# Optimization experiments

Hardware: AMD Instinct MI355X
Metric: run time of the kernel (lower is better)

Reference implementation:

```python
import jax, jax.numpy as jnp
import numpy as np

B, C, H, W = 8, 256, 128, 128
KC, VC, HEADS = 256, 256, 8


def setup_inputs() -> dict:
    key = jax.random.key(0)
    ks = jax.random.split(key, 10)
    s = 0.05
    return {
        "x": jax.random.normal(ks[0], (B, C, H, W), jnp.float32),
        "Wk": jax.random.normal(ks[1], (KC, C), jnp.float32) * s,
        "bk": jax.random.normal(ks[2], (KC,), jnp.float32) * s,
        "Wq": jax.random.normal(ks[3], (KC, C), jnp.float32) * s,
        "bq": jax.random.normal(ks[4], (KC,), jnp.float32) * s,
        "Wv": jax.random.normal(ks[5], (VC, C), jnp.float32) * s,
        "bv": jax.random.normal(ks[6], (VC,), jnp.float32) * s,
        "Wr": jax.random.normal(ks[7], (C, VC), jnp.float32) * s,
        "br": jax.random.normal(ks[8], (C,), jnp.float32) * s,
        "head_count": HEADS,
    }


def reference(x, Wk, bk, Wq, bq, Wv, bv, Wr, br, head_count):
    n, c, h, w = x.shape
    hw = h * w
    xf = x.reshape(n, c, hw)  # [n, C, S]
    # 1x1 convs == per-pixel linear projections
    keys = jnp.einsum('kc,ncs->nks', Wk, xf) + bk[None, :, None]
    queries = jnp.einsum('kc,ncs->nks', Wq, xf) + bq[None, :, None]
    values = jnp.einsum('vc,ncs->nvs', Wv, xf) + bv[None, :, None]

    dk = Wk.shape[0] // head_count
    dv = Wv.shape[0] // head_count
    # split heads along channel dim (matches torch channel slicing)
    K = jax.nn.softmax(keys.reshape(n, head_count, dk, hw), axis=-1)   # softmax over spatial
    Q = jax.nn.softmax(queries.reshape(n, head_count, dk, hw), axis=2) # softmax over key dim
    V = values.reshape(n, head_count, dv, hw)

    # context = K @ V^T : [n, h, dk, dv]
    ctx = jnp.einsum('nhks,nhvs->nhkv', K, V)
    # attended = ctx^T @ Q : [n, h, dv, S]
    att = jnp.einsum('nhkv,nhks->nhvs', ctx, Q).reshape(n, head_count * dv, h, w)

    attention = jnp.einsum('ov,nvhw->nohw', Wr, att) + br[None, :, None, None]
    # attention map: per-head mean over key dim, then mean over heads
    attention_map = K.mean(axis=2).mean(axis=1).reshape(n, h, w)
    # torch returns the LAST head's context (loop variable after the loop)
    context_last = ctx[:, -1]
    return attention, context_last, attention_map
```

## Files before the change

### kernel.cpp

```cpp
#include <hip/hip_runtime.h>
#include <hip/hip_bf16.h>

typedef float f32x4 __attribute__((ext_vector_type(4)));
typedef short s16x8 __attribute__((ext_vector_type(8)));
typedef short s16x4 __attribute__((ext_vector_type(4)));
typedef __bf16 bf16x8 __attribute__((ext_vector_type(8)));
typedef unsigned short u16;

#define DEVI __device__ __forceinline__

static constexpr int    HW      = 16384;
static constexpr size_t BSTRIDE = (size_t)256 * HW;

static constexpr size_t oXBT   = 0;
static constexpr size_t oEK    = oXBT  + (size_t)8 * HW * 256 * 2;
static constexpr size_t oQT    = oEK   + (size_t)8 * 256 * HW * 2;
static constexpr size_t oVB    = oQT   + (size_t)8 * HW * 256 * 2;
static constexpr size_t oWK    = oVB   + (size_t)8 * 256 * HW * 2;
static constexpr size_t oBIAS  = oWK   + (size_t)768 * 256 * 2;
static constexpr size_t oISE   = oBIAS + 4096;
static constexpr size_t oPS    = oISE  + 8192;
static constexpr size_t oCTX   = oPS   + (size_t)256 * 2048 * 4;
static constexpr size_t oMB    = oCTX  + (size_t)64 * 1024 * 4;
static constexpr size_t oCPART = oMB   + (size_t)8 * 256 * 256 * 2;
static constexpr size_t oMPART = oCPART + (size_t)4096 * 1024 * 4;

DEVI float bf2f(short x) {
  unsigned u = ((unsigned)(unsigned short)x) << 16;
  return __builtin_bit_cast(float, u);
}
DEVI u16 f2bf(float x) { return __builtin_bit_cast(u16, (__bf16)x); }

DEVI void gld16(const void* g, void* l) {
  __builtin_amdgcn_global_load_lds(
      (__attribute__((address_space(1))) void*)(g),
      (__attribute__((address_space(3))) void*)(l), 16, 0, 0);
}

__global__ __launch_bounds__(256) void k_pt(
    const float* __restrict__ x,
    const float* __restrict__ Wk, const float* __restrict__ Wq, const float* __restrict__ Wv,
    const float* __restrict__ bk, const float* __restrict__ bq, const float* __restrict__ bv,
    u16* __restrict__ xbT, u16* __restrict__ Wkqv, float* __restrict__ bias)
{
  __shared__ u16 lds[64 * 256];
  const int t = threadIdx.x;
  const int tb = blockIdx.x;
  if (tb < 2048) {
    const int n = tb >> 8;
    const int s0 = (tb & 255) * 64;
    const float* src = x + ((size_t)n * 256 + t) * HW + s0;
    #pragma unroll
    for (int i = 0; i < 16; ++i) {
      f32x4 v = *(const f32x4*)(src + i * 4);
      #pragma unroll
      for (int j = 0; j < 4; ++j) lds[(i * 4 + j) * 256 + t] = f2bf(v[j]);
    }
    __syncthreads();
    s16x8* gp = (s16x8*)(xbT + (size_t)n * BSTRIDE + (size_t)s0 * 256);
    const s16x8* lp = (const s16x8*)lds;
    #pragma unroll
    for (int i = 0; i < 8; ++i) gp[t + i * 256] = lp[t + i * 256];
  } else {
    const int i = (tb - 2048) * 256 + t;
    for (int p = i; p < 768 * 256; p += 64 * 256) {
      float v = (p < 65536) ? Wk[p] : (p < 131072 ? Wq[p - 65536] : Wv[p - 131072]);
      Wkqv[p] = f2bf(v);
    }
    if (i < 768) bias[i] = (i < 256) ? bk[i] : (i < 512 ? bq[i - 256] : bv[i - 512]);
  }
}

__global__ __launch_bounds__(256, 2) void k_proj3(
    const u16* __restrict__ W, const u16* __restrict__ xbT, const float* __restrict__ bias,
    u16* __restrict__ ek, u16* __restrict__ qT, u16* __restrict__ vb, float* __restrict__ ps)
{
  __shared__ u16 smem[40960];
  const int t = threadIdx.x;
  const int L = blockIdx.x;
  const int n = L & 7;
  const int idx = L >> 3;
  const int mh = idx & 1;
  const int sb = idx >> 1;
  const int m0 = mh * 128;
  const int s0 = sb * 128;
  const int lane = t & 63;
  const int l15 = lane & 15, l4 = (lane >> 4) & 3;
  const int wv = t >> 6;
  const int wm = (wv & 1) * 64, wn = (wv >> 1) * 64;

  const u16* Bb = xbT + (size_t)n * BSTRIDE + (size_t)s0 * 256;

  float bK[4], bV[4];
  #pragma unroll
  for (int mf = 0; mf < 4; ++mf) {
    bK[mf] = bias[m0 + wm + mf * 16 + l15];
    bV[mf] = bias[512 + m0 + wm + mf * 16 + l15];
  }

  #pragma unroll
  for (int i = 0; i < 16; ++i) {
    const int f = i * 256 + t;
    const int row = f >> 5, c = f & 31;
    gld16(Bb + (size_t)row * 256 + ((c ^ (row & 7)) * 8), smem + f * 8);
  }

  auto STAGEA = [&](int g) {
    const int kt = g & 7;
    const int op = g >> 3;
    const int wr0 = (op == 0) ? 0 : (op == 1 ? 512 : 256);
    const u16* Ab = W + (size_t)(wr0 + m0) * 256;
    #pragma unroll
    for (int i = 0; i < 2; ++i) {
      const int f = i * 256 + t;
      const int row = f >> 2, c = f & 3;
      gld16(Ab + (size_t)row * 256 + kt * 32 + ((c ^ (row & 3)) * 8),
            smem + 32768 + (g & 1) * 4096 + f * 8);
    }
  };

  STAGEA(0); STAGEA(1);

  f32x4 acc[4][4] = {};
  u16* ekb = ek + (size_t)n * BSTRIDE;
  u16* vbb = vb + (size_t)n * BSTRIDE;

  #pragma unroll
  for (int g = 0; g < 24; ++g) {
    if (g == 23) asm volatile("s_waitcnt vmcnt(0)" ::: "memory");
    else         asm volatile("s_waitcnt vmcnt(2)" ::: "memory");
    __builtin_amdgcn_s_barrier();

    const int kt = g & 7;
    bf16x8 af[4], bff[4];
    #pragma unroll
    for (int gg = 0; gg < 4; ++gg) {
      const int mrow = wm + gg * 16 + l15;
      const int srow = wn + gg * 16 + l15;
      const int cidx = kt * 4 + l4;
      af[gg]  = *(const bf16x8*)&smem[32768 + (g & 1) * 4096 + mrow * 32 + ((l4 ^ (mrow & 3)) * 8)];
      bff[gg] = *(const bf16x8*)&smem[srow * 256 + ((cidx ^ (srow & 7)) * 8)];
    }
    __builtin_amdgcn_s_setprio(1);
    if (g < 16) {
      #pragma unroll
      for (int sf = 0; sf < 4; ++sf)
        #pragma unroll
        for (int mf = 0; mf < 4; ++mf)
          acc[sf][mf] = __builtin_amdgcn_mfma_f32_16x16x32_bf16(bff[sf], af[mf], acc[sf][mf], 0, 0, 0);
    } else {
      #pragma unroll
      for (int mg = 0; mg < 4; ++mg)
        #pragma unroll
        for (int ng = 0; ng < 4; ++ng)
          acc[mg][ng] = __builtin_amdgcn_mfma_f32_16x16x32_bf16(af[mg], bff[ng], acc[mg][ng], 0, 0, 0);
    }
    __builtin_amdgcn_s_setprio(0);

    asm volatile("s_waitcnt lgkmcnt(0)" ::: "memory");
    __builtin_amdgcn_s_barrier();
    if (g < 22) STAGEA(g + 2);

    if (g == 7) {
      float rs[4] = {0.f, 0.f, 0.f, 0.f};
      #pragma unroll
      for (int sf = 0; sf < 4; ++sf)
        #pragma unroll
        for (int mf = 0; mf < 4; ++mf) {
          s16x4 pk;
          #pragma unroll
          for (int r = 0; r < 4; ++r) {
            const float e = __expf(acc[sf][mf][r] + bK[mf]);
            rs[mf] += e;
            pk[r] = (short)f2bf(e);
          }
          *(s16x4*)(ekb + (size_t)(m0 + wm + mf * 16 + l15) * HW + s0 + wn + sf * 16 + l4 * 4) = pk;
        }
      #pragma unroll
      for (int mf = 0; mf < 4; ++mf) {
        float v = rs[mf];
        v += __shfl_xor(v, 16); v += __shfl_xor(v, 32);
        if (l4 == 0)
          ps[((size_t)(sb * 2 + (wn >> 6))) * 2048 + n * 256 + m0 + wm + mf * 16 + l15] = v;
      }
      #pragma unroll
      for (int sf = 0; sf < 4; ++sf)
        #pragma unroll
        for (int mf = 0; mf < 4; ++mf) acc[sf][mf] = f32x4{0.f, 0.f, 0.f, 0.f};
    } else if (g == 15) {
      #pragma unroll
      for (int sf = 0; sf < 4; ++sf)
        #pragma unroll
        for (int mf = 0; mf < 4; ++mf) {
          s16x4 pk;
          #pragma unroll
          for (int r = 0; r < 4; ++r) pk[r] = (short)f2bf(acc[sf][mf][r] + bV[mf]);
          *(s16x4*)(vbb + (size_t)(m0 + wm + mf * 16 + l15) * HW + s0 + wn + sf * 16 + l4 * 4) = pk;
        }
      #pragma unroll
      for (int sf = 0; sf < 4; ++sf)
        #pragma unroll
        for (int mf = 0; mf < 4; ++mf) acc[sf][mf] = f32x4{0.f, 0.f, 0.f, 0.f};
    }
  }

  #pragma unroll
  for (int mg = 0; mg < 4; ++mg)
    #pragma unroll
    for (int r = 0; r < 4; ++r) {
      const float bb = bias[256 + m0 + wm + mg * 16 + l4 * 4 + r];
      #pragma unroll
      for (int ng = 0; ng < 4; ++ng) acc[mg][ng][r] += bb;
    }
  #pragma unroll
  for (int hh = 0; hh < 2; ++hh)
    #pragma unroll
    for (int ng = 0; ng < 4; ++ng) {
      float s = 0.f;
      #pragma unroll
      for (int mg = hh * 2; mg < hh * 2 + 2; ++mg)
        #pragma unroll
        for (int r = 0; r < 4; ++r) { const float e = __expf(acc[mg][ng][r]); acc[mg][ng][r] = e; s += e; }
      s += __shfl_xor(s, 16);
      s += __shfl_xor(s, 32);
      const float inv = 1.f / s;
      #pragma unroll
      for (int mg = hh * 2; mg < hh * 2 + 2; ++mg)
        #pragma unroll
        for (int r = 0; r < 4; ++r) acc[mg][ng][r] *= inv;
    }
  __syncthreads();
  #pragma unroll
  for (int mg = 0; mg < 4; ++mg)
    #pragma unroll
    for (int ng = 0; ng < 4; ++ng)
      #pragma unroll
      for (int r = 0; r < 4; ++r) {
        const int srow = wn + ng * 16 + l15;
        const int mcol = wm + mg * 16 + l4 * 4 + r;
        smem[srow * 136 + mcol] = f2bf(acc[mg][ng][r]);
      }
  __syncthreads();
  u16* O = qT + (size_t)n * BSTRIDE + (size_t)s0 * 256 + mh * 128;
  #pragma unroll
  for (int it = 0; it < 8; ++it) {
    const int row = it * 16 + (t >> 4);
    *(s16x8*)(O + (size_t)row * 256 + (t & 15) * 8) = *(const s16x8*)&smem[row * 136 + (t & 15) * 8];
  }
}

__global__ __launch_bounds__(256) void k_inv(const float* __restrict__ ps, float* __restrict__ ise)
{
  const int i = blockIdx.x * 256 + threadIdx.x;
  float s = 0.f;
  for (int b = 0; b < 256; ++b) s += ps[(size_t)b * 2048 + i];
  ise[i] = 1.f / s;
}

__global__ __launch_bounds__(64) void k_ctx_part(
    const u16* __restrict__ ek, const u16* __restrict__ vb, const float* __restrict__ ise,
    float* __restrict__ cpart, float* __restrict__ mpart)
{
  const int blk = blockIdx.x;
  const int chunk = blk & 63, nh = blk >> 6;
  const int h = nh & 7, n = nh >> 3;
  const int lane = threadIdx.x;
  const int l15 = lane & 15, l4 = lane >> 4;
  const u16* kb = ek + ((size_t)n * 256 + h * 32) * HW;
  const u16* vv = vb + ((size_t)n * 256 + h * 32) * HW;
  const float iv0 = ise[n * 256 + h * 32 + l15];
  const float iv1 = ise[n * 256 + h * 32 + 16 + l15];
  f32x4 acc[2][2] = {};
  float macc[8][8] = {};
  const int sbase = chunk * 256 + l4 * 8;
  #pragma unroll
  for (int ks = 0; ks < 8; ++ks) {
    const int sb = sbase + ks * 32;
    bf16x8 ef[2], vf[2];
    #pragma unroll
    for (int g = 0; g < 2; ++g) {
      ef[g] = *(const bf16x8*)(kb + (size_t)(g * 16 + l15) * HW + sb);
      vf[g] = *(const bf16x8*)(vv + (size_t)(g * 16 + l15) * HW + sb);
    }
    #pragma unroll
    for (int j = 0; j < 8; ++j)
      macc[ks][j] = fmaf(iv0, (float)ef[0][j], fmaf(iv1, (float)ef[1][j], macc[ks][j]));
    #pragma unroll
    for (int a = 0; a < 2; ++a)
      #pragma unroll
      for (int b = 0; b < 2; ++b)
        acc[a][b] = __builtin_amdgcn_mfma_f32_16x16x32_bf16(ef[a], vf[b], acc[a][b], 0, 0, 0);
  }
  float* op = cpart + (size_t)blk * 1024;
  #pragma unroll
  for (int a = 0; a < 2; ++a)
    #pragma unroll
    for (int b = 0; b < 2; ++b)
      #pragma unroll
      for (int r = 0; r < 4; ++r)
        op[(a * 16 + l4 * 4 + r) * 32 + b * 16 + l15] = acc[a][b][r];
  #pragma unroll
  for (int ks = 0; ks < 8; ++ks)
    #pragma unroll
    for (int j = 0; j < 8; ++j) {
      float v = macc[ks][j];
      v += __shfl_xor(v, 1); v += __shfl_xor(v, 2);
      v += __shfl_xor(v, 4); v += __shfl_xor(v, 8);
      macc[ks][j] = v;
    }
  if (l15 == 0) {
    float* mp = mpart + ((size_t)h * 8 + n) * HW + sbase;
    #pragma unroll
    for (int ks = 0; ks < 8; ++ks) {
      f32x4 a = {macc[ks][0], macc[ks][1], macc[ks][2], macc[ks][3]};
      f32x4 b = {macc[ks][4], macc[ks][5], macc[ks][6], macc[ks][7]};
      *(f32x4*)(mp + ks * 32)     = a;
      *(f32x4*)(mp + ks * 32 + 4) = b;
    }
  }
}

__global__ __launch_bounds__(256) void k_post(
    const float* __restrict__ cpart, const float* __restrict__ ise,
    const float* __restrict__ Wr, const float* __restrict__ mpart,
    u16* __restrict__ Mb, float* __restrict__ dctx, float* __restrict__ dmap)
{
  const int t = threadIdx.x;
  if (blockIdx.x < 64) {
    const int nh = blockIdx.x, n = nh >> 3, h = nh & 7;
    __shared__ float cl[1024];
    f32x4 a = {};
    for (int c = 0; c < 64; ++c) a += *(const f32x4*)(cpart + ((size_t)nh * 64 + c) * 1024 + t * 4);
    const float inv = ise[n * 256 + h * 32 + (t >> 3)];
    a *= inv;
    *(f32x4*)(cl + t * 4) = a;
    if (h == 7) *(f32x4*)(dctx + (size_t)n * 1024 + t * 4) = a;
    __syncthreads();
    const int o = t;
    float wr[32];
    const float* wp = Wr + (size_t)o * 256 + h * 32;
    #pragma unroll
    for (int v = 0; v < 32; ++v) wr[v] = wp[v];
    u16* mp = Mb + ((size_t)n * 256 + o) * 256 + h * 32;
    #pragma unroll 4
    for (int k = 0; k < 32; ++k) {
      float s = 0.f;
      #pragma unroll
      for (int v = 0; v < 32; ++v) s += wr[v] * cl[k * 32 + v];
      mp[k] = f2bf(s);
    }
  } else {
    const int i = (blockIdx.x - 64) * 256 + t;
    f32x4 a = {};
    #pragma unroll
    for (int h = 0; h < 8; ++h) a += *(const f32x4*)(mpart + (size_t)h * 131072 + (size_t)i * 4);
    a *= (1.0f / 256.0f);
    *(f32x4*)(dmap + (size_t)i * 4) = a;
  }
}

__global__ __launch_bounds__(256, 2) void k_attn2(
    const u16* __restrict__ Mb, const u16* __restrict__ qT, const float* __restrict__ br,
    float* __restrict__ Out)
{
  __shared__ u16 smem[32768];
  const int t = threadIdx.x;
  const int L = blockIdx.x;
  const int n = L & 7;
  const int idx = L >> 3;
  const int mb = idx & 1;
  const int sq = idx >> 1;
  const int m0 = mb * 128;
  const int lane = t & 63;
  const int l15 = lane & 15, l4 = (lane >> 4) & 3;
  const int wv = t >> 6;
  const int wm = (wv & 1) * 64, wn = (wv >> 1) * 64;
  const u16* Ab = Mb + (size_t)n * 65536 + (size_t)m0 * 256;
  const u16* Bb = qT + (size_t)n * BSTRIDE;
  u16* Al = smem;
  u16* Bl = smem + 16384;

  float biasv[4];
  #pragma unroll
  for (int mf = 0; mf < 4; ++mf) biasv[mf] = br[m0 + wm + mf * 16 + l15];

  const int rr = t >> 3;
  const int csh = t & 7;
  auto STAGE = [&](int buf, int it) {
    const int k0 = (it & 3) * 64;
    const size_t s_t0 = (size_t)((sq * 4 + (it >> 2)) * 128);
    #pragma unroll
    for (int i = 0; i < 4; ++i) {
      const int row = i * 32 + rr;
      const int cs = (csh ^ (row & 7)) * 8;
      gld16(Ab + (size_t)row * 256 + k0 + cs,  Al + buf * 8192 + i * 2048 + t * 8);
      gld16(Bb + (s_t0 + row) * 256 + k0 + cs, Bl + buf * 8192 + i * 2048 + t * 8);
    }
  };

  f32x4 acc[4][4] = {};
  STAGE(0, 0); STAGE(1, 1);

  float* ob = Out + (size_t)n * BSTRIDE;

  #pragma unroll
  for (int it = 0; it < 16; ++it) {
    if (it == 15)                          asm volatile("s_waitcnt vmcnt(0)" ::: "memory");
    else if ((it & 3) <= 1 && it >= 4)     asm volatile("s_waitcnt vmcnt(24)" ::: "memory");
    else                                   asm volatile("s_waitcnt vmcnt(8)" ::: "memory");
    __builtin_amdgcn_s_barrier();

    const int buf = it & 1;
    #pragma unroll
    for (int ks = 0; ks < 2; ++ks) {
      bf16x8 af[4], bff[4];
      #pragma unroll
      for (int g = 0; g < 4; ++g) {
        const int mrow = wm + g * 16 + l15;
        const int srow = wn + g * 16 + l15;
        af[g]  = *(const bf16x8*)&Al[buf * 8192 + mrow * 64 + (((ks * 4 + l4) ^ (mrow & 7)) * 8)];
        bff[g] = *(const bf16x8*)&Bl[buf * 8192 + srow * 64 + (((ks * 4 + l4) ^ (srow & 7)) * 8)];
      }
      __builtin_amdgcn_s_setprio(1);
      #pragma unroll
      for (int sf = 0; sf < 4; ++sf)
        #pragma unroll
        for (int mf = 0; mf < 4; ++mf)
          acc[sf][mf] = __builtin_amdgcn_mfma_f32_16x16x32_bf16(bff[sf], af[mf], acc[sf][mf], 0, 0, 0);
      __builtin_amdgcn_s_setprio(0);
    }
    asm volatile("s_waitcnt lgkmcnt(0)" ::: "memory");
    __builtin_amdgcn_s_barrier();
    if (it < 14) STAGE(buf, it + 2);

    if ((it & 3) == 3) {
      const int s0t = (sq * 4 + (it >> 2)) * 128;
      #pragma unroll
      for (int sf = 0; sf < 4; ++sf)
        #pragma unroll
        for (int mf = 0; mf < 4; ++mf) {
          f32x4 o = acc[sf][mf] + biasv[mf];
          *(f32x4*)(ob + (size_t)(m0 + wm + mf * 16 + l15) * HW + s0t + wn + sf * 16 + l4 * 4) = o;
          acc[sf][mf] = f32x4{0.f, 0.f, 0.f, 0.f};
        }
    }
  }
}

extern "C" void kernel_launch(void* const* d_in, const int* in_sizes, int n_in,
                              void* d_out, int out_size, void* d_ws, size_t ws_size,
                              hipStream_t stream)
{
  (void)in_sizes; (void)n_in; (void)out_size; (void)ws_size;
  const float* x  = (const float*)d_in[0];
  const float* Wk = (const float*)d_in[1];
  const float* bk = (const float*)d_in[2];
  const float* Wq = (const float*)d_in[3];
  const float* bq = (const float*)d_in[4];
  const float* Wv = (const float*)d_in[5];
  const float* bv = (const float*)d_in[6];
  const float* Wr = (const float*)d_in[7];
  const float* br = (const float*)d_in[8];

  char* ws = (char*)d_ws;
  u16*   xbT  = (u16*)(ws + oXBT);
  u16*   ek   = (u16*)(ws + oEK);
  u16*   qT   = (u16*)(ws + oQT);
  u16*   vb   = (u16*)(ws + oVB);
  u16*   Wkqv = (u16*)(ws + oWK);
  float* bias = (float*)(ws + oBIAS);
  float* ise  = (float*)(ws + oISE);
  float* ps   = (float*)(ws + oPS);
  u16*   Mb   = (u16*)(ws + oMB);
  float* cpart= (float*)(ws + oCPART);
  float* mpart= (float*)(ws + oMPART);

  float* attn = (float*)d_out;
  float* dctx = (float*)d_out + 33554432;
  float* dmap = (float*)d_out + 33562624;

  k_pt<<<2112, 256, 0, stream>>>(x, Wk, Wq, Wv, bk, bq, bv, xbT, Wkqv, bias);
  k_proj3<<<2048, 256, 0, stream>>>(Wkqv, xbT, bias, ek, qT, vb, ps);
  k_inv<<<8, 256, 0, stream>>>(ps, ise);
  k_ctx_part<<<4096, 64, 0, stream>>>(ek, vb, ise, cpart, mpart);
  k_post<<<192, 256, 0, stream>>>(cpart, ise, Wr, mpart, Mb, dctx, dmap);
  k_attn2<<<512, 256, 0, stream>>>(Mb, qT, br, attn);
}
```

Before: 274.3 us.

## Fuse x fp32-to-bf16 transpose into projection kernel, drop xbT buffer

The separate pass that converted x to bf16 and transposed it into a workspace buffer is removed. The projection kernel now reads fp32 x directly, converts it, and writes it transposed and swizzled into shared memory. This saves a full write and re-read of the 64MB intermediate. The weight swizzle in LDS is also changed to reduce bank conflicts. The trade-off is that each block now does synchronous, non-async fp32 global loads with scattered 2-byte LDS stores, and both M-halves of a block read the same x tile, so x is loaded twice.

```diff
diff --git a/kernel.cpp b/kernel.cpp
--- a/kernel.cpp
+++ b/kernel.cpp
@@ -37,42 +37,22 @@
       (__attribute__((address_space(3))) void*)(l), 16, 0, 0);
 }
 
-__global__ __launch_bounds__(256) void k_pt(
-    const float* __restrict__ x,
+__global__ __launch_bounds__(256) void k_prep(
     const float* __restrict__ Wk, const float* __restrict__ Wq, const float* __restrict__ Wv,
     const float* __restrict__ bk, const float* __restrict__ bq, const float* __restrict__ bv,
-    u16* __restrict__ xbT, u16* __restrict__ Wkqv, float* __restrict__ bias)
-{
-  __shared__ u16 lds[64 * 256];
-  const int t = threadIdx.x;
-  const int tb = blockIdx.x;
-  if (tb < 2048) {
-    const int n = tb >> 8;
-    const int s0 = (tb & 255) * 64;
-    const float* src = x + ((size_t)n * 256 + t) * HW + s0;
-    #pragma unroll
-    for (int i = 0; i < 16; ++i) {
-      f32x4 v = *(const f32x4*)(src + i * 4);
-      #pragma unroll
-      for (int j = 0; j < 4; ++j) lds[(i * 4 + j) * 256 + t] = f2bf(v[j]);
-    }
-    __syncthreads();
-    s16x8* gp = (s16x8*)(xbT + (size_t)n * BSTRIDE + (size_t)s0 * 256);
-    const s16x8* lp = (const s16x8*)lds;
-    #pragma unroll
-    for (int i = 0; i < 8; ++i) gp[t + i * 256] = lp[t + i * 256];
-  } else {
-    const int i = (tb - 2048) * 256 + t;
-    for (int p = i; p < 768 * 256; p += 64 * 256) {
-      float v = (p < 65536) ? Wk[p] : (p < 131072 ? Wq[p - 65536] : Wv[p - 131072]);
-      Wkqv[p] = f2bf(v);
-    }
-    if (i < 768) bias[i] = (i < 256) ? bk[i] : (i < 512 ? bq[i - 256] : bv[i - 512]);
-  }
-}
-
-__global__ __launch_bounds__(256, 2) void k_proj3(
-    const u16* __restrict__ W, const u16* __restrict__ xbT, const float* __restrict__ bias,
+    u16* __restrict__ Wkqv, float* __restrict__ bias)
+{
+  int i = blockIdx.x * 256 + threadIdx.x;
+  for (int p = i; p < 768 * 256; p += 64 * 256) {
+    float v = (p < 65536) ? Wk[p] : (p < 131072 ? Wq[p - 65536] : Wv[p - 131072]);
+    Wkqv[p] = f2bf(v);
+  }
+  if (i < 768) bias[i] = (i < 256) ? bk[i] : (i < 512 ? bq[i - 256] : bv[i - 512]);
+}
+
+__global__ __launch_bounds__(256, 2) void k_projX(
+    const float* __restrict__ x,
+    const u16* __restrict__ W, const float* __restrict__ bias,
     u16* __restrict__ ek, u16* __restrict__ qT, u16* __restrict__ vb, float* __restrict__ ps)
 {
   __shared__ u16 smem[40960];
@@ -89,8 +69,6 @@
   const int wv = t >> 6;
   const int wm = (wv & 1) * 64, wn = (wv >> 1) * 64;
 
-  const u16* Bb = xbT + (size_t)n * BSTRIDE + (size_t)s0 * 256;
-
   float bK[4], bV[4];
   #pragma unroll
   for (int mf = 0; mf < 4; ++mf) {
@@ -98,12 +76,20 @@
     bV[mf] = bias[512 + m0 + wm + mf * 16 + l15];
   }
 
-  #pragma unroll
-  for (int i = 0; i < 16; ++i) {
-    const int f = i * 256 + t;
-    const int row = f >> 5, c = f & 31;
-    gld16(Bb + (size_t)row * 256 + ((c ^ (row & 7)) * 8), smem + f * 8);
-  }
+  {
+    const float* xr = x + ((size_t)n * 256 + t) * HW + s0;
+    const int ch = t >> 3, cw = t & 7;
+    #pragma unroll
+    for (int i = 0; i < 32; ++i) {
+      f32x4 v = *(const f32x4*)(xr + i * 4);
+      #pragma unroll
+      for (int j = 0; j < 4; ++j) {
+        const int s = i * 4 + j;
+        smem[s * 256 + ((ch ^ (s & 7)) * 8) + cw] = f2bf(v[j]);
+      }
+    }
+  }
+  __syncthreads();
 
   auto STAGEA = [&](int g) {
     const int kt = g & 7;
@@ -114,7 +100,8 @@
     for (int i = 0; i < 2; ++i) {
       const int f = i * 256 + t;
       const int row = f >> 2, c = f & 3;
-      gld16(Ab + (size_t)row * 256 + kt * 32 + ((c ^ (row & 3)) * 8),
+      const int fa = (row & 3) ^ ((row >> 2) & 3);
+      gld16(Ab + (size_t)row * 256 + kt * 32 + ((c ^ fa) * 8),
             smem + 32768 + (g & 1) * 4096 + f * 8);
     }
   };
@@ -138,7 +125,8 @@
       const int mrow = wm + gg * 16 + l15;
       const int srow = wn + gg * 16 + l15;
       const int cidx = kt * 4 + l4;
-      af[gg]  = *(const bf16x8*)&smem[32768 + (g & 1) * 4096 + mrow * 32 + ((l4 ^ (mrow & 3)) * 8)];
+      const int fa = (mrow & 3) ^ ((mrow >> 2) & 3);
+      af[gg]  = *(const bf16x8*)&smem[32768 + (g & 1) * 4096 + mrow * 32 + ((l4 ^ fa) * 8)];
       bff[gg] = *(const bf16x8*)&smem[srow * 256 + ((cidx ^ (srow & 7)) * 8)];
     }
     __builtin_amdgcn_s_setprio(1);
@@ -463,7 +451,6 @@
   const float* br = (const float*)d_in[8];
 
   char* ws = (char*)d_ws;
-  u16*   xbT  = (u16*)(ws + oXBT);
   u16*   ek   = (u16*)(ws + oEK);
   u16*   qT   = (u16*)(ws + oQT);
   u16*   vb   = (u16*)(ws + oVB);
@@ -479,8 +466,8 @@
   float* dctx = (float*)d_out + 33554432;
   float* dmap = (float*)d_out + 33562624;
 
-  k_pt<<<2112, 256, 0, stream>>>(x, Wk, Wq, Wv, bk, bq, bv, xbT, Wkqv, bias);
-  k_proj3<<<2048, 256, 0, stream>>>(Wkqv, xbT, bias, ek, qT, vb, ps);
+  k_prep<<<64, 256, 0, stream>>>(Wk, Wq, Wv, bk, bq, bv, Wkqv, bias);
+  k_projX<<<2048, 256, 0, stream>>>(x, Wkqv, bias, ek, qT, vb, ps);
   k_inv<<<8, 256, 0, stream>>>(ps, ise);
   k_ctx_part<<<4096, 64, 0, stream>>>(ek, vb, ise, cpart, mpart);
   k_post<<<192, 256, 0, stream>>>(cpart, ise, Wr, mpart, Mb, dctx, dmap);
```

Result: faster. 266.5 us (-2.8%).
